# Optimization experiments

Measured on AMD Instinct MI355X. Metric: run time of the kernel, lower is better.

The kernel has to match this reference:

```python
import jax, jax.numpy as jnp
import numpy as np

VOCAB, DEC_VOCAB, E, H, T = 256, 128, 1024, 2048, 1025

def setup_inputs() -> dict:
    key = jax.random.key(0)
    ks = jax.random.split(key, 8)
    return {
        "x": jax.random.randint(ks[0], (T,), 0, VOCAB),
        "len_words": T - 1,  # scalar python int
        "enc_emb": jax.random.normal(ks[1], (VOCAB, E), jnp.float32) * 0.02,
        "enc_w_ih": jax.random.normal(ks[2], (3 * H, E), jnp.float32) * 0.02,
        "enc_w_hh": jax.random.normal(ks[3], (3 * H, H), jnp.float32) * 0.02,
        "enc_b_ih": jax.random.normal(ks[4], (3 * H,), jnp.float32) * 0.02,
        "enc_b_hh": jax.random.normal(ks[5], (3 * H,), jnp.float32) * 0.02,
        "dec_emb": jax.random.normal(ks[6], (DEC_VOCAB, E), jnp.float32) * 0.02,
    }

def _gru_scan(xs, w_ih, w_hh, b_ih, b_hh):
    # xs: [T, 1, E]; returns final hidden [1, H]
    h_dim = w_hh.shape[1]
    def cell(h, xt):
        rzn_ih = xt @ w_ih.T + b_ih            # [1, 3H]
        rzn_hh = h @ w_hh.T + b_hh             # [1, 3H]
        rz = jax.nn.sigmoid(rzn_ih[:, :2 * h_dim] + rzn_hh[:, :2 * h_dim])
        r, z = rz[:, :h_dim], rz[:, h_dim:]
        n = jnp.tanh(rzn_ih[:, 2 * h_dim:] + r * rzn_hh[:, 2 * h_dim:])
        h = (1.0 - z) * n + z * h
        return h, None
    h0 = jnp.zeros((1, h_dim), jnp.float32)
    h_last, _ = jax.lax.scan(cell, h0, xs)
    return h_last

def reference(x, len_words, enc_emb, enc_w_ih, enc_w_hh, enc_b_ih, enc_b_hh, dec_emb):
    steps = int(len_words) + 1
    emb = enc_emb[x[:steps]]                   # [steps, E]
    xs = emb[:, None, :]                       # [steps, 1, E] (batch 1)
    h = _gru_scan(xs, enc_w_ih, enc_w_hh, enc_b_ih, enc_b_hh)  # [1, H]
    dec = dec_emb[2][None, None, :]            # [1, 1, E]
    return dec, h
```

## Files before the change

### kernel.cpp

```cpp
#include <hip/hip_runtime.h>
#include <hip/hip_bf16.h>
#include <math.h>

#define E_DIM 1024
#define H_DIM 2048
#define H3 6144
#define VOCAB 256
#define NCOMP 256
#define TPW 512

typedef unsigned long long u64;
typedef unsigned int u32;
typedef u32 u32x4 __attribute__((ext_vector_type(4)));

__global__ __launch_bounds__(256) void ih_table_kernel(
    const float* __restrict__ emb, const float* __restrict__ w_ih,
    const float* __restrict__ b_ih, float* __restrict__ table)
{
    __shared__ float As[32][65];
    __shared__ float Bs[32][65];
    const int v0 = blockIdx.y * 64;
    const int j0 = blockIdx.x * 64;
    const int t  = threadIdx.x;
    const int tx = t % 16, ty = t / 16;
    const int lr0 = t / 8;
    const int lc  = (t % 8) * 4;
    float acc[4][4] = {};

    for (int k0 = 0; k0 < E_DIM; k0 += 32) {
        __syncthreads();
#pragma unroll
        for (int p = 0; p < 2; ++p) {
            int r = lr0 + p * 32;
            float4 a = *(const float4*)(emb  + (size_t)(v0 + r) * E_DIM + k0 + lc);
            As[lc+0][r] = a.x; As[lc+1][r] = a.y; As[lc+2][r] = a.z; As[lc+3][r] = a.w;
            float4 b = *(const float4*)(w_ih + (size_t)(j0 + r) * E_DIM + k0 + lc);
            Bs[lc+0][r] = b.x; Bs[lc+1][r] = b.y; Bs[lc+2][r] = b.z; Bs[lc+3][r] = b.w;
        }
        __syncthreads();
#pragma unroll 8
        for (int kk = 0; kk < 32; ++kk) {
            float a4[4], b4[4];
#pragma unroll
            for (int i = 0; i < 4; ++i) a4[i] = As[kk][ty * 4 + i];
#pragma unroll
            for (int i = 0; i < 4; ++i) b4[i] = Bs[kk][tx * 4 + i];
#pragma unroll
            for (int i = 0; i < 4; ++i)
#pragma unroll
                for (int j = 0; j < 4; ++j) acc[i][j] += a4[i] * b4[j];
        }
    }
    const int j = j0 + tx * 4;
    float4 bias = *(const float4*)(b_ih + j);
#pragma unroll
    for (int i = 0; i < 4; ++i) {
        int v = v0 + ty * 4 + i;
        float4 o;
        o.x = acc[i][0] + bias.x; o.y = acc[i][1] + bias.y;
        o.z = acc[i][2] + bias.z; o.w = acc[i][3] + bias.w;
        *(float4*)(table + (size_t)v * H3 + j) = o;
    }
}

__global__ __launch_bounds__(TPW, 2) void gru_persistent(
    const int* __restrict__ x, const int* __restrict__ lenp,
    const float* __restrict__ w_hh, const float* __restrict__ b_hh,
    const float* __restrict__ table,
    u64* hbuf0, u64* hbuf1)
{
    __shared__ float hsh[2][H_DIM];
    const int cw   = blockIdx.x;
    const int tid  = threadIdx.x;
    const int base = cw * 8;
    const int uu   = tid >> 6;
    const int l    = tid & 63;
    const int S    = lenp[0] + 1;

    float4 wv[3][8];
#pragma unroll
    for (int g = 0; g < 3; ++g) {
        const float4* wr =
            (const float4*)(w_hh + (size_t)(g * H_DIM + base + uu) * H_DIM);
#pragma unroll
        for (int i = 0; i < 8; ++i) wv[g][i] = wr[i * 64 + l];
    }
#pragma unroll
    for (int g = 0; g < 3; ++g)
#pragma unroll
        for (int i = 0; i < 8; ++i)
            asm volatile("" : "+v"(wv[g][i].x), "+v"(wv[g][i].y),
                              "+v"(wv[g][i].z), "+v"(wv[g][i].w));

    float bhr = 0.f, bhz = 0.f, bhn = 0.f;
    if (l == 0) {
        bhr = b_hh[base + uu];
        bhz = b_hh[H_DIM + base + uu];
        bhn = b_hh[2 * H_DIM + base + uu];
    }

    u64* bufs[2] = {hbuf0, hbuf1};

    for (int s = 0; s < S; ++s) {
        const u64* src = bufs[s & 1];
        u64*       dst = bufs[(s + 1) & 1];
        float*     hs  = hsh[s & 1];

        float ihr = 0.f, ihz = 0.f, ihn = 0.f;
        if (l == 0) {
            const float* trow = table + (size_t)x[s] * H3;
            ihr = trow[base + uu];
            ihz = trow[H_DIM + base + uu];
            ihn = trow[2 * H_DIM + base + uu];
        }

        {
            const unsigned want = (unsigned)s;
            const u64* ps = src + 4 * tid;
            u32x4 a, b;
            asm volatile("global_load_dwordx4 %0, %2, off sc0 sc1\n\t"
                         "global_load_dwordx4 %1, %3, off sc0 sc1\n\t"
                         "s_waitcnt vmcnt(0)"
                         : "=&v"(a), "=&v"(b)
                         : "v"(ps), "v"(ps + 2)
                         : "memory");
            for (;;) {
                bool ok = (a.y == want) & (a.w == want) &
                          (b.y == want) & (b.w == want);
                if (ok) break;
                __builtin_amdgcn_s_sleep(4);
                asm volatile("global_load_dwordx4 %0, %2, off sc0 sc1\n\t"
                             "global_load_dwordx4 %1, %3, off sc0 sc1\n\t"
                             "s_waitcnt vmcnt(0)"
                             : "=&v"(a), "=&v"(b)
                             : "v"(ps), "v"(ps + 2)
                             : "memory");
            }
            float4 st;
            st.x = __uint_as_float(a.x);
            st.y = __uint_as_float(a.z);
            st.z = __uint_as_float(b.x);
            st.w = __uint_as_float(b.z);
            *(float4*)(hs + 4 * tid) = st;
        }
        __syncthreads();

        const float4* h4 = (const float4*)hs;
        float4 ar = make_float4(0.f, 0.f, 0.f, 0.f);
        float4 az = make_float4(0.f, 0.f, 0.f, 0.f);
        float4 an = make_float4(0.f, 0.f, 0.f, 0.f);
#pragma unroll
        for (int i = 0; i < 8; ++i) {
            float4 hv = h4[i * 64 + l];
            ar.x += wv[0][i].x * hv.x; ar.y += wv[0][i].y * hv.y;
            ar.z += wv[0][i].z * hv.z; ar.w += wv[0][i].w * hv.w;
            az.x += wv[1][i].x * hv.x; az.y += wv[1][i].y * hv.y;
            az.z += wv[1][i].z * hv.z; az.w += wv[1][i].w * hv.w;
            an.x += wv[2][i].x * hv.x; an.y += wv[2][i].y * hv.y;
            an.z += wv[2][i].z * hv.z; an.w += wv[2][i].w * hv.w;
        }
        float pr = (ar.x + ar.y) + (ar.z + ar.w);
        float pz = (az.x + az.y) + (az.z + az.w);
        float pn = (an.x + an.y) + (an.z + an.w);
#pragma unroll
        for (int d = 1; d < 64; d <<= 1) {
            pr += __shfl_xor(pr, d);
            pz += __shfl_xor(pz, d);
            pn += __shfl_xor(pn, d);
        }

        if (l == 0) {
            float hprev = hs[base + uu];
            float hr = pr + bhr;
            float hz = pz + bhz;
            float hn = pn + bhn;
            float r_ = 1.f / (1.f + __expf(-(ihr + hr)));
            float z_ = 1.f / (1.f + __expf(-(ihz + hz)));
            float xn = ihn + r_ * hn;
            float axn = fabsf(xn), te = __expf(2.f * axn);
            float n_ = copysignf(1.f - 2.f / (te + 1.f), xn);
            float hnew = (1.f - z_) * n_ + z_ * hprev;
            u64 pack = ((u64)(unsigned)(s + 1) << 32) |
                       (u64)__float_as_uint(hnew);
            __hip_atomic_store(dst + base + uu, pack, __ATOMIC_RELAXED,
                               __HIP_MEMORY_SCOPE_AGENT);
        }
    }
}

__global__ void epilogue_kernel(const int* __restrict__ lenp,
                                const float* __restrict__ dec_emb,
                                const u64* __restrict__ hbuf0,
                                const u64* __restrict__ hbuf1,
                                float* __restrict__ out)
{
    int i = blockIdx.x * blockDim.x + threadIdx.x;
    int S = lenp[0] + 1;
    const u64* hb = (S & 1) ? hbuf1 : hbuf0;
    if (i < E_DIM) out[i] = dec_emb[2 * E_DIM + i];
    else if (i < E_DIM + H_DIM)
        out[i] = __uint_as_float((unsigned)hb[i - E_DIM]);
}

extern "C" void kernel_launch(void* const* d_in, const int* in_sizes, int n_in,
                              void* d_out, int out_size, void* d_ws, size_t ws_size,
                              hipStream_t stream) {
    const int*   x       = (const int*)d_in[0];
    const int*   lenp    = (const int*)d_in[1];
    const float* emb     = (const float*)d_in[2];
    const float* w_ih    = (const float*)d_in[3];
    const float* w_hh    = (const float*)d_in[4];
    const float* b_ih    = (const float*)d_in[5];
    const float* b_hh    = (const float*)d_in[6];
    const float* dec_emb = (const float*)d_in[7];
    float* out = (float*)d_out;

    char* ws = (char*)d_ws;
    float* table = (float*)ws;
    u64*   hbuf0 = (u64*)(ws + (size_t)VOCAB * H3 * 4);
    u64*   hbuf1 = hbuf0 + H_DIM;

    hipMemsetAsync(hbuf0, 0, (size_t)2 * H_DIM * sizeof(u64), stream);

    dim3 gA(H3 / 64, VOCAB / 64);
    ih_table_kernel<<<gA, 256, 0, stream>>>(emb, w_ih, b_ih, table);

    gru_persistent<<<dim3(NCOMP), dim3(TPW), 0, stream>>>(
        x, lenp, w_hh, b_hh, table, hbuf0, hbuf1);

    epilogue_kernel<<<12, 256, 0, stream>>>(lenp, dec_emb, hbuf0, hbuf1, out);
}
```

Measured before the change: 2.469 ms.

## Add per-XCD hub blocks that mirror hidden state for local polling

The first block to arrive on each XCD becomes a hub. Only the hub polls the global hidden-state buffer with device-coherent loads, then copies what it reads into a per-XCD mirror. The other blocks poll that mirror with loads that can be served from the shared L2, and fall back to global polling after 16 misses. Sleep intervals are also shortened. The goal is to cut cross-XCD coherent traffic at each recurrent step, at the cost of an extra hop through the hub. The mirrors are never cleared between calls, so a leftover tag from a previous run could be mistaken for fresh data.

```diff
diff --git a/kernel.cpp b/kernel.cpp
--- a/kernel.cpp
+++ b/kernel.cpp
@@ -8,6 +8,7 @@
 #define VOCAB 256
 #define NCOMP 256
 #define TPW 512
+#define NXCD 8
 
 typedef unsigned long long u64;
 typedef unsigned int u32;
@@ -67,9 +68,11 @@
     const int* __restrict__ x, const int* __restrict__ lenp,
     const float* __restrict__ w_hh, const float* __restrict__ b_hh,
     const float* __restrict__ table,
-    u64* hbuf0, u64* hbuf1)
+    u64* hbuf0, u64* hbuf1, u64* mirrors, u32* hubcnt)
 {
     __shared__ float hsh[2][H_DIM];
+    __shared__ int   hubSh;
+    __shared__ u64*  mirSh;
     const int cw   = blockIdx.x;
     const int tid  = threadIdx.x;
     const int base = cw * 8;
@@ -77,6 +80,18 @@
     const int l    = tid & 63;
     const int S    = lenp[0] + 1;
 
+    if (tid == 0) {
+        u32 xcc;
+        asm volatile("s_getreg_b32 %0, hwreg(HW_REG_XCC_ID)" : "=s"(xcc));
+        xcc &= (NXCD - 1);
+        u32 prev = atomicAdd(&hubcnt[xcc], 1u);
+        hubSh = (prev == 0);
+        mirSh = mirrors + (size_t)xcc * 2 * H_DIM;
+    }
+    __syncthreads();
+    const bool isHub = (hubSh != 0);
+    u64* const mir   = mirSh;
+
     float4 wv[3][8];
 #pragma unroll
     for (int g = 0; g < 3; ++g) {
@@ -102,9 +117,10 @@
     u64* bufs[2] = {hbuf0, hbuf1};
 
     for (int s = 0; s < S; ++s) {
-        const u64* src = bufs[s & 1];
-        u64*       dst = bufs[(s + 1) & 1];
-        float*     hs  = hsh[s & 1];
+        const u64* src  = bufs[s & 1];
+        u64*       dst  = bufs[(s + 1) & 1];
+        u64*       msrc = mir + (size_t)(s & 1) * H_DIM;
+        float*     hs   = hsh[s & 1];
 
         float ihr = 0.f, ihz = 0.f, ihn = 0.f;
         if (l == 0) {
@@ -114,35 +130,63 @@
             ihn = trow[2 * H_DIM + base + uu];
         }
 
-        {
-            const unsigned want = (unsigned)s;
+        const unsigned want = (unsigned)s;
+        u32x4 a, b;
+
+        if (isHub) {
             const u64* ps = src + 4 * tid;
-            u32x4 a, b;
-            asm volatile("global_load_dwordx4 %0, %2, off sc0 sc1\n\t"
-                         "global_load_dwordx4 %1, %3, off sc0 sc1\n\t"
-                         "s_waitcnt vmcnt(0)"
-                         : "=&v"(a), "=&v"(b)
-                         : "v"(ps), "v"(ps + 2)
-                         : "memory");
             for (;;) {
-                bool ok = (a.y == want) & (a.w == want) &
-                          (b.y == want) & (b.w == want);
-                if (ok) break;
-                __builtin_amdgcn_s_sleep(4);
-                asm volatile("global_load_dwordx4 %0, %2, off sc0 sc1\n\t"
-                             "global_load_dwordx4 %1, %3, off sc0 sc1\n\t"
-                             "s_waitcnt vmcnt(0)"
-                             : "=&v"(a), "=&v"(b)
-                             : "v"(ps), "v"(ps + 2)
-                             : "memory");
+                asm volatile(
+                    "global_load_dwordx4 %0, %2, off sc0 sc1\n\t"
+                    "global_load_dwordx4 %1, %2, off offset:16 sc0 sc1\n\t"
+                    "s_waitcnt vmcnt(0)"
+                    : "=&v"(a), "=&v"(b)
+                    : "v"(ps)
+                    : "memory");
+                if ((a.y == want) & (a.w == want) &
+                    (b.y == want) & (b.w == want)) break;
+                __builtin_amdgcn_s_sleep(1);
             }
-            float4 st;
-            st.x = __uint_as_float(a.x);
-            st.y = __uint_as_float(a.z);
-            st.z = __uint_as_float(b.x);
-            st.w = __uint_as_float(b.z);
-            *(float4*)(hs + 4 * tid) = st;
-        }
+            u32x4* mp = (u32x4*)(msrc + 4 * tid);
+            mp[0] = a;
+            mp[1] = b;
+        } else {
+            const u64* ps = msrc + 4 * tid;
+            const u64* gp = src + 4 * tid;
+            int misses = 0;
+            bool done = false;
+            while (!done && misses < 16) {
+                asm volatile(
+                    "global_load_dwordx4 %0, %2, off sc0\n\t"
+                    "global_load_dwordx4 %1, %2, off offset:16 sc0\n\t"
+                    "s_waitcnt vmcnt(0)"
+                    : "=&v"(a), "=&v"(b)
+                    : "v"(ps)
+                    : "memory");
+                done = (a.y == want) & (a.w == want) &
+                       (b.y == want) & (b.w == want);
+                if (!done) { ++misses; __builtin_amdgcn_s_sleep(1); }
+            }
+            while (!done) {
+                asm volatile(
+                    "global_load_dwordx4 %0, %2, off sc0 sc1\n\t"
+                    "global_load_dwordx4 %1, %2, off offset:16 sc0 sc1\n\t"
+                    "s_waitcnt vmcnt(0)"
+                    : "=&v"(a), "=&v"(b)
+                    : "v"(gp)
+                    : "memory");
+                done = (a.y == want) & (a.w == want) &
+                       (b.y == want) & (b.w == want);
+                if (!done) __builtin_amdgcn_s_sleep(2);
+            }
+        }
+
+        float4 st;
+        st.x = __uint_as_float(a.x);
+        st.y = __uint_as_float(a.z);
+        st.z = __uint_as_float(b.x);
+        st.w = __uint_as_float(b.z);
+        *(float4*)(hs + 4 * tid) = st;
         __syncthreads();
 
         const float4* h4 = (const float4*)hs;
@@ -216,17 +260,21 @@
     float* out = (float*)d_out;
 
     char* ws = (char*)d_ws;
-    float* table = (float*)ws;
-    u64*   hbuf0 = (u64*)(ws + (size_t)VOCAB * H3 * 4);
-    u64*   hbuf1 = hbuf0 + H_DIM;
-
-    hipMemsetAsync(hbuf0, 0, (size_t)2 * H_DIM * sizeof(u64), stream);
+    float* table  = (float*)ws;
+    u64*   hbuf0  = (u64*)(ws + (size_t)VOCAB * H3 * 4);
+    u64*   hbuf1  = hbuf0 + H_DIM;
+    u32*   hubcnt = (u32*)(hbuf1 + H_DIM);
+    u64*   mirrors = (u64*)(ws + (size_t)VOCAB * H3 * 4 + 33024);
+
+    hipMemsetAsync(hbuf0, 0,
+                   (size_t)2 * H_DIM * sizeof(u64) + NXCD * sizeof(u32),
+                   stream);
 
     dim3 gA(H3 / 64, VOCAB / 64);
     ih_table_kernel<<<gA, 256, 0, stream>>>(emb, w_ih, b_ih, table);
 
     gru_persistent<<<dim3(NCOMP), dim3(TPW), 0, stream>>>(
-        x, lenp, w_hh, b_hh, table, hbuf0, hbuf1);
+        x, lenp, w_hh, b_hh, table, hbuf0, hbuf1, mirrors, hubcnt);
 
     epilogue_kernel<<<12, 256, 0, stream>>>(lenp, dec_emb, hbuf0, hbuf1, out);
 }
```

New measurement: 5.300 ms. +114.7%, slower.

## Halve persistent GRU blocks by giving each wave two hidden units

Applied to the files above, without the earlier changes.

Each wave now holds the recurrent weights for two hidden units in registers, so a block covers 16 units and only 128 persistent blocks run instead of 256. The aim is to cut the number of blocks that poll the global hidden-state buffer and the synchronisation fan-in each step, and to publish both units with a single 16-byte store. The cost is doubled register footprint per thread (two 96-float weight sets), which risks spills or lower occupancy. Per-wave compute per step also doubles, lengthening the serial critical path.

```diff
diff --git a/kernel.cpp b/kernel.cpp
--- a/kernel.cpp
+++ b/kernel.cpp
@@ -6,8 +6,9 @@
 #define H_DIM 2048
 #define H3 6144
 #define VOCAB 256
-#define NCOMP 256
+#define NCOMP 128
 #define TPW 512
+#define UPW 16
 
 typedef unsigned long long u64;
 typedef unsigned int u32;
@@ -72,31 +73,36 @@
     __shared__ float hsh[2][H_DIM];
     const int cw   = blockIdx.x;
     const int tid  = threadIdx.x;
-    const int base = cw * 8;
+    const int base = cw * UPW;
     const int uu   = tid >> 6;
     const int l    = tid & 63;
     const int S    = lenp[0] + 1;
-
-    float4 wv[3][8];
+    const int myu  = base + 2 * uu + (l & 1);
+
+    float4 wva[3][8], wvb[3][8];
 #pragma unroll
     for (int g = 0; g < 3; ++g) {
-        const float4* wr =
-            (const float4*)(w_hh + (size_t)(g * H_DIM + base + uu) * H_DIM);
-#pragma unroll
-        for (int i = 0; i < 8; ++i) wv[g][i] = wr[i * 64 + l];
+        const float4* ra =
+            (const float4*)(w_hh + (size_t)(g * H_DIM + base + 2 * uu) * H_DIM);
+        const float4* rb = ra + (H_DIM / 4);
+#pragma unroll
+        for (int i = 0; i < 8; ++i) { wva[g][i] = ra[i * 64 + l]; wvb[g][i] = rb[i * 64 + l]; }
     }
 #pragma unroll
     for (int g = 0; g < 3; ++g)
 #pragma unroll
-        for (int i = 0; i < 8; ++i)
-            asm volatile("" : "+v"(wv[g][i].x), "+v"(wv[g][i].y),
-                              "+v"(wv[g][i].z), "+v"(wv[g][i].w));
+        for (int i = 0; i < 8; ++i) {
+            asm volatile("" : "+v"(wva[g][i].x), "+v"(wva[g][i].y),
+                              "+v"(wva[g][i].z), "+v"(wva[g][i].w));
+            asm volatile("" : "+v"(wvb[g][i].x), "+v"(wvb[g][i].y),
+                              "+v"(wvb[g][i].z), "+v"(wvb[g][i].w));
+        }
 
     float bhr = 0.f, bhz = 0.f, bhn = 0.f;
-    if (l == 0) {
-        bhr = b_hh[base + uu];
-        bhz = b_hh[H_DIM + base + uu];
-        bhn = b_hh[2 * H_DIM + base + uu];
+    if (l < 2) {
+        bhr = b_hh[myu];
+        bhz = b_hh[H_DIM + myu];
+        bhn = b_hh[2 * H_DIM + myu];
     }
 
     u64* bufs[2] = {hbuf0, hbuf1};
@@ -107,22 +113,23 @@
         float*     hs  = hsh[s & 1];
 
         float ihr = 0.f, ihz = 0.f, ihn = 0.f;
-        if (l == 0) {
+        if (l < 2) {
             const float* trow = table + (size_t)x[s] * H3;
-            ihr = trow[base + uu];
-            ihz = trow[H_DIM + base + uu];
-            ihn = trow[2 * H_DIM + base + uu];
-        }
+            ihr = trow[myu];
+            ihz = trow[H_DIM + myu];
+            ihn = trow[2 * H_DIM + myu];
+        }
+
+        const unsigned want = (unsigned)s;
 
         {
-            const unsigned want = (unsigned)s;
             const u64* ps = src + 4 * tid;
             u32x4 a, b;
             asm volatile("global_load_dwordx4 %0, %2, off sc0 sc1\n\t"
-                         "global_load_dwordx4 %1, %3, off sc0 sc1\n\t"
+                         "global_load_dwordx4 %1, %2, off offset:16 sc0 sc1\n\t"
                          "s_waitcnt vmcnt(0)"
                          : "=&v"(a), "=&v"(b)
-                         : "v"(ps), "v"(ps + 2)
+                         : "v"(ps)
                          : "memory");
             for (;;) {
                 bool ok = (a.y == want) & (a.w == want) &
@@ -130,10 +137,10 @@
                 if (ok) break;
                 __builtin_amdgcn_s_sleep(4);
                 asm volatile("global_load_dwordx4 %0, %2, off sc0 sc1\n\t"
-                             "global_load_dwordx4 %1, %3, off sc0 sc1\n\t"
+                             "global_load_dwordx4 %1, %2, off offset:16 sc0 sc1\n\t"
                              "s_waitcnt vmcnt(0)"
                              : "=&v"(a), "=&v"(b)
-                             : "v"(ps), "v"(ps + 2)
+                             : "v"(ps)
                              : "memory");
             }
             float4 st;
@@ -146,44 +153,76 @@
         __syncthreads();
 
         const float4* h4 = (const float4*)hs;
+
         float4 ar = make_float4(0.f, 0.f, 0.f, 0.f);
         float4 az = make_float4(0.f, 0.f, 0.f, 0.f);
         float4 an = make_float4(0.f, 0.f, 0.f, 0.f);
 #pragma unroll
         for (int i = 0; i < 8; ++i) {
             float4 hv = h4[i * 64 + l];
-            ar.x += wv[0][i].x * hv.x; ar.y += wv[0][i].y * hv.y;
-            ar.z += wv[0][i].z * hv.z; ar.w += wv[0][i].w * hv.w;
-            az.x += wv[1][i].x * hv.x; az.y += wv[1][i].y * hv.y;
-            az.z += wv[1][i].z * hv.z; az.w += wv[1][i].w * hv.w;
-            an.x += wv[2][i].x * hv.x; an.y += wv[2][i].y * hv.y;
-            an.z += wv[2][i].z * hv.z; an.w += wv[2][i].w * hv.w;
-        }
-        float pr = (ar.x + ar.y) + (ar.z + ar.w);
-        float pz = (az.x + az.y) + (az.z + az.w);
-        float pn = (an.x + an.y) + (an.z + an.w);
+            ar.x += wva[0][i].x * hv.x; ar.y += wva[0][i].y * hv.y;
+            ar.z += wva[0][i].z * hv.z; ar.w += wva[0][i].w * hv.w;
+            az.x += wva[1][i].x * hv.x; az.y += wva[1][i].y * hv.y;
+            az.z += wva[1][i].z * hv.z; az.w += wva[1][i].w * hv.w;
+            an.x += wva[2][i].x * hv.x; an.y += wva[2][i].y * hv.y;
+            an.z += wva[2][i].z * hv.z; an.w += wva[2][i].w * hv.w;
+        }
+        float prA = (ar.x + ar.y) + (ar.z + ar.w);
+        float pzA = (az.x + az.y) + (az.z + az.w);
+        float pnA = (an.x + an.y) + (an.z + an.w);
 #pragma unroll
         for (int d = 1; d < 64; d <<= 1) {
-            pr += __shfl_xor(pr, d);
-            pz += __shfl_xor(pz, d);
-            pn += __shfl_xor(pn, d);
-        }
-
+            prA += __shfl_xor(prA, d);
+            pzA += __shfl_xor(pzA, d);
+            pnA += __shfl_xor(pnA, d);
+        }
+
+        ar = make_float4(0.f, 0.f, 0.f, 0.f);
+        az = make_float4(0.f, 0.f, 0.f, 0.f);
+        an = make_float4(0.f, 0.f, 0.f, 0.f);
+#pragma unroll
+        for (int i = 0; i < 8; ++i) {
+            float4 hv = h4[i * 64 + l];
+            ar.x += wvb[0][i].x * hv.x; ar.y += wvb[0][i].y * hv.y;
+            ar.z += wvb[0][i].z * hv.z; ar.w += wvb[0][i].w * hv.w;
+            az.x += wvb[1][i].x * hv.x; az.y += wvb[1][i].y * hv.y;
+            az.z += wvb[1][i].z * hv.z; az.w += wvb[1][i].w * hv.w;
+            an.x += wvb[2][i].x * hv.x; an.y += wvb[2][i].y * hv.y;
+            an.z += wvb[2][i].z * hv.z; an.w += wvb[2][i].w * hv.w;
+        }
+        float prB = (ar.x + ar.y) + (ar.z + ar.w);
+        float pzB = (az.x + az.y) + (az.z + az.w);
+        float pnB = (an.x + an.y) + (an.z + an.w);
+#pragma unroll
+        for (int d = 1; d < 64; d <<= 1) {
+            prB += __shfl_xor(prB, d);
+            pzB += __shfl_xor(pzB, d);
+            pnB += __shfl_xor(pnB, d);
+        }
+
+        const bool isB = (l & 1);
+        float pr = isB ? prB : prA;
+        float pz = isB ? pzB : pzA;
+        float pn = isB ? pnB : pnA;
+        float hprev = hs[base + 2 * uu + (l & 1)];
+        float hr = pr + bhr;
+        float hz = pz + bhz;
+        float hn = pn + bhn;
+        float r_ = 1.f / (1.f + __expf(-(ihr + hr)));
+        float z_ = 1.f / (1.f + __expf(-(ihz + hz)));
+        float xn = ihn + r_ * hn;
+        float axn = fabsf(xn), te = __expf(2.f * axn);
+        float n_ = copysignf(1.f - 2.f / (te + 1.f), xn);
+        float hnew = (1.f - z_) * n_ + z_ * hprev;
+
+        float hB = __shfl(hnew, 1);
         if (l == 0) {
-            float hprev = hs[base + uu];
-            float hr = pr + bhr;
-            float hz = pz + bhz;
-            float hn = pn + bhn;
-            float r_ = 1.f / (1.f + __expf(-(ihr + hr)));
-            float z_ = 1.f / (1.f + __expf(-(ihz + hz)));
-            float xn = ihn + r_ * hn;
-            float axn = fabsf(xn), te = __expf(2.f * axn);
-            float n_ = copysignf(1.f - 2.f / (te + 1.f), xn);
-            float hnew = (1.f - z_) * n_ + z_ * hprev;
-            u64 pack = ((u64)(unsigned)(s + 1) << 32) |
-                       (u64)__float_as_uint(hnew);
-            __hip_atomic_store(dst + base + uu, pack, __ATOMIC_RELAXED,
-                               __HIP_MEMORY_SCOPE_AGENT);
+            u32x4 pk;
+            pk.x = __float_as_uint(hnew); pk.y = (u32)(s + 1);
+            pk.z = __float_as_uint(hB);   pk.w = (u32)(s + 1);
+            u64* dp = dst + base + 2 * uu;
+            asm volatile("global_store_dwordx4 %0, %1, off sc0 sc1"
+                         :: "v"(dp), "v"(pk) : "memory");
         }
     }
 }
```

Result: slower. 4.618 ms (+87.0%).

## Replace block barrier with per-wave LDS flags and split dot product by quarter

Applied to the files above, without the earlier changes.

Replaces the per-step __syncthreads with per-wave LDS flags. Each wave publishes that it has stored its slice of h, and consumers wait only for the waves that wrote the half of h they read first, then for the other half. This lets waves start the matvec on partial data instead of waiting at a full barrier. The two global loads now share one address register with an immediate offset. The change relies on the monotonic flag ordering and on correct LDS memory-ordering semantics. It also adds spin polling on LDS.

```diff
diff --git a/kernel.cpp b/kernel.cpp
--- a/kernel.cpp
+++ b/kernel.cpp
@@ -70,6 +70,7 @@
     u64* hbuf0, u64* hbuf1)
 {
     __shared__ float hsh[2][H_DIM];
+    __shared__ int   wflags[8];
     const int cw   = blockIdx.x;
     const int tid  = threadIdx.x;
     const int base = cw * 8;
@@ -99,6 +100,9 @@
         bhn = b_hh[2 * H_DIM + base + uu];
     }
 
+    if (tid < 8) wflags[tid] = -1;
+    __syncthreads();
+
     u64* bufs[2] = {hbuf0, hbuf1};
 
     for (int s = 0; s < S; ++s) {
@@ -114,15 +118,16 @@
             ihn = trow[2 * H_DIM + base + uu];
         }
 
+        const unsigned want = (unsigned)s;
+
         {
-            const unsigned want = (unsigned)s;
             const u64* ps = src + 4 * tid;
             u32x4 a, b;
             asm volatile("global_load_dwordx4 %0, %2, off sc0 sc1\n\t"
-                         "global_load_dwordx4 %1, %3, off sc0 sc1\n\t"
+                         "global_load_dwordx4 %1, %2, off offset:16 sc0 sc1\n\t"
                          "s_waitcnt vmcnt(0)"
                          : "=&v"(a), "=&v"(b)
-                         : "v"(ps), "v"(ps + 2)
+                         : "v"(ps)
                          : "memory");
             for (;;) {
                 bool ok = (a.y == want) & (a.w == want) &
@@ -130,10 +135,10 @@
                 if (ok) break;
                 __builtin_amdgcn_s_sleep(4);
                 asm volatile("global_load_dwordx4 %0, %2, off sc0 sc1\n\t"
-                             "global_load_dwordx4 %1, %3, off sc0 sc1\n\t"
+                             "global_load_dwordx4 %1, %2, off offset:16 sc0 sc1\n\t"
                              "s_waitcnt vmcnt(0)"
                              : "=&v"(a), "=&v"(b)
-                             : "v"(ps), "v"(ps + 2)
+                             : "v"(ps)
                              : "memory");
             }
             float4 st;
@@ -143,14 +148,30 @@
             st.w = __uint_as_float(b.z);
             *(float4*)(hs + 4 * tid) = st;
         }
-        __syncthreads();
+        asm volatile("s_waitcnt lgkmcnt(0)" ::: "memory");
+        if (l == 0)
+            __hip_atomic_store(&wflags[uu], s, __ATOMIC_RELEASE,
+                               __HIP_MEMORY_SCOPE_WORKGROUP);
 
         const float4* h4 = (const float4*)hs;
         float4 ar = make_float4(0.f, 0.f, 0.f, 0.f);
         float4 az = make_float4(0.f, 0.f, 0.f, 0.f);
         float4 an = make_float4(0.f, 0.f, 0.f, 0.f);
-#pragma unroll
-        for (int i = 0; i < 8; ++i) {
+
+        for (;;) {
+            int f0 = __hip_atomic_load(&wflags[0], __ATOMIC_ACQUIRE,
+                                       __HIP_MEMORY_SCOPE_WORKGROUP);
+            int f1 = __hip_atomic_load(&wflags[1], __ATOMIC_ACQUIRE,
+                                       __HIP_MEMORY_SCOPE_WORKGROUP);
+            int f2 = __hip_atomic_load(&wflags[2], __ATOMIC_ACQUIRE,
+                                       __HIP_MEMORY_SCOPE_WORKGROUP);
+            int f3 = __hip_atomic_load(&wflags[3], __ATOMIC_ACQUIRE,
+                                       __HIP_MEMORY_SCOPE_WORKGROUP);
+            if ((f0 >= s) & (f1 >= s) & (f2 >= s) & (f3 >= s)) break;
+            __builtin_amdgcn_s_sleep(1);
+        }
+#pragma unroll
+        for (int i = 0; i < 4; ++i) {
             float4 hv = h4[i * 64 + l];
             ar.x += wv[0][i].x * hv.x; ar.y += wv[0][i].y * hv.y;
             ar.z += wv[0][i].z * hv.z; ar.w += wv[0][i].w * hv.w;
@@ -159,6 +180,30 @@
             an.x += wv[2][i].x * hv.x; an.y += wv[2][i].y * hv.y;
             an.z += wv[2][i].z * hv.z; an.w += wv[2][i].w * hv.w;
         }
+
+        for (;;) {
+            int f4 = __hip_atomic_load(&wflags[4], __ATOMIC_ACQUIRE,
+                                       __HIP_MEMORY_SCOPE_WORKGROUP);
+            int f5 = __hip_atomic_load(&wflags[5], __ATOMIC_ACQUIRE,
+                                       __HIP_MEMORY_SCOPE_WORKGROUP);
+            int f6 = __hip_atomic_load(&wflags[6], __ATOMIC_ACQUIRE,
+                                       __HIP_MEMORY_SCOPE_WORKGROUP);
+            int f7 = __hip_atomic_load(&wflags[7], __ATOMIC_ACQUIRE,
+                                       __HIP_MEMORY_SCOPE_WORKGROUP);
+            if ((f4 >= s) & (f5 >= s) & (f6 >= s) & (f7 >= s)) break;
+            __builtin_amdgcn_s_sleep(1);
+        }
+#pragma unroll
+        for (int i = 4; i < 8; ++i) {
+            float4 hv = h4[i * 64 + l];
+            ar.x += wv[0][i].x * hv.x; ar.y += wv[0][i].y * hv.y;
+            ar.z += wv[0][i].z * hv.z; ar.w += wv[0][i].w * hv.w;
+            az.x += wv[1][i].x * hv.x; az.y += wv[1][i].y * hv.y;
+            az.z += wv[1][i].z * hv.z; az.w += wv[1][i].w * hv.w;
+            an.x += wv[2][i].x * hv.x; an.y += wv[2][i].y * hv.y;
+            an.z += wv[2][i].z * hv.z; an.w += wv[2][i].w * hv.w;
+        }
+
         float pr = (ar.x + ar.y) + (ar.z + ar.w);
         float pz = (az.x + az.y) + (az.z + az.w);
         float pn = (an.x + an.y) + (an.z + an.w);
```

Measured after the change: 2.979 ms. +20.7%, slower.
